# Kernel optimization log

Measured on AMD Instinct MI355X. Metric: run time of the kernel, lower is better.

## Reference

```python
import jax, jax.numpy as jnp
import numpy as np

M, K, N = 8192, 4096, 4096

def setup_inputs() -> dict:
    key = jax.random.key(0)
    k1, k2, k3, k4 = jax.random.split(key, 4)
    x = jax.random.normal(k1, (M, K), dtype=jnp.float32)
    # pre-quantized int8 weights [K, N] and per-output-channel scales [N]
    weight_q = jax.random.randint(k2, (K, N), -128, 128, dtype=jnp.int32).astype(jnp.int8)
    weight_scale = (jax.random.uniform(k3, (N,), dtype=jnp.float32) * 0.01 + 1e-4)
    bias = jax.random.normal(k4, (N,), dtype=jnp.float32) * 0.02
    return {"x": x, "weight_q": weight_q, "weight_scale": weight_scale, "bias": bias}

def reference(x, weight_q, weight_scale, bias):
    # dynamic per-row int8 quantization of activations
    max_vals = jnp.max(jnp.abs(x), axis=-1, keepdims=True)          # [M, 1]
    a_scale = jnp.maximum(max_vals / 127.0, 1e-8)                    # [M, 1]
    x_q = jnp.clip(jnp.round(x / a_scale), -128, 127).astype(jnp.int8)
    c = jnp.matmul(x_q.astype(jnp.float32), weight_q.astype(jnp.float32))  # [M, N]
    # dequantize: per-row activation scale * per-column weight scale
    c = c * a_scale * weight_scale[None, :]
    out = c.astype(x.dtype) + bias
    return out
```

## Files before the change

### kernel.cpp

```cpp
#include <hip/hip_runtime.h>


typedef int int32x4 __attribute__((ext_vector_type(4)));

#define TILE_BM 256
#define TILE_BN 256
#define TILE_BK 128

__device__ __forceinline__ void async_copy16(const void* g, void* l) {
    __builtin_amdgcn_global_load_lds(
        (const __attribute__((address_space(1))) unsigned int*)g,
        (__attribute__((address_space(3))) unsigned int*)l,
        16, 0, 0);
}

__device__ __forceinline__ int quant1(float x, float s) {
    float q = rintf(x / s);
    q = fminf(127.0f, fmaxf(-128.0f, q));
    return (int)q;
}

__global__ __launch_bounds__(256) void quant_kernel(
    const float* __restrict__ x, signed char* __restrict__ xq,
    float* __restrict__ ascale, int K)
{
    const int row = blockIdx.x;
    const int t = threadIdx.x;
    const float4* xr4 = (const float4*)(x + (size_t)row * K);

    float4 v[4];
    float mx = 0.0f;
#pragma unroll
    for (int i = 0; i < 4; ++i) {
        v[i] = xr4[i * 256 + t];
        mx = fmaxf(mx, fmaxf(fmaxf(fabsf(v[i].x), fabsf(v[i].y)),
                             fmaxf(fabsf(v[i].z), fabsf(v[i].w))));
    }
#pragma unroll
    for (int off = 32; off > 0; off >>= 1)
        mx = fmaxf(mx, __shfl_xor(mx, off, 64));
    __shared__ float wmax[4];
    if ((t & 63) == 0) wmax[t >> 6] = mx;
    __syncthreads();
    mx = fmaxf(fmaxf(wmax[0], wmax[1]), fmaxf(wmax[2], wmax[3]));

    const float s = fmaxf(mx / 127.0f, 1e-8f);
    if (t == 0) ascale[row] = s;

    int* xqr = (int*)(xq + (size_t)row * K);
#pragma unroll
    for (int i = 0; i < 4; ++i) {
        const int b0 = quant1(v[i].x, s);
        const int b1 = quant1(v[i].y, s);
        const int b2 = quant1(v[i].z, s);
        const int b3 = quant1(v[i].w, s);
        xqr[i * 256 + t] = (b0 & 255) | ((b1 & 255) << 8) | ((b2 & 255) << 16) | ((b3 & 255) << 24);
    }
}

__global__ __launch_bounds__(256) void transpose_pack_kernel(
    const int* __restrict__ Bq, signed char* __restrict__ Bt, int K, int N)
{
    __shared__ int lds[64 * 17];
    const int t = threadIdx.x;
    const int n0 = blockIdx.x * 64;
    const int k0 = blockIdx.y * 64;

    const int r = t >> 4;
    const int ncol = (t & 15) * 4;

    const int* src = Bq + (size_t)(k0 + 4 * r) * N + n0 + ncol;
    const int4 u0 = *(const int4*)(src);
    const int4 u1 = *(const int4*)(src + N);
    const int4 u2 = *(const int4*)(src + 2 * (size_t)N);
    const int4 u3 = *(const int4*)(src + 3 * (size_t)N);

    lds[(ncol + 0) * 17 + r] = (u0.x & 255) | ((u1.x & 255) << 8) | ((u2.x & 255) << 16) | ((u3.x & 255) << 24);
    lds[(ncol + 1) * 17 + r] = (u0.y & 255) | ((u1.y & 255) << 8) | ((u2.y & 255) << 16) | ((u3.y & 255) << 24);
    lds[(ncol + 2) * 17 + r] = (u0.z & 255) | ((u1.z & 255) << 8) | ((u2.z & 255) << 16) | ((u3.z & 255) << 24);
    lds[(ncol + 3) * 17 + r] = (u0.w & 255) | ((u1.w & 255) << 8) | ((u2.w & 255) << 16) | ((u3.w & 255) << 24);
    __syncthreads();

    const int nl = t >> 2, ch = t & 3;
    int o[4];
#pragma unroll
    for (int i = 0; i < 4; ++i) o[i] = lds[nl * 17 + ch * 4 + i];
    *(int32x4*)(Bt + (size_t)(n0 + nl) * K + k0 + ch * 16) = *(const int32x4*)o;
}


#define SBAR() do { asm volatile("" ::: "memory"); __builtin_amdgcn_s_barrier(); asm volatile("" ::: "memory"); } while (0)
#define LGKM0() asm volatile("s_waitcnt lgkmcnt(0)" ::: "memory")
#define VMCNT(n) asm volatile("s_waitcnt vmcnt(" #n ")" ::: "memory")

#define MFMA_Q(AF, MB, NB)                                                              \
    do {                                                                                \
        __builtin_amdgcn_s_setprio(1);                                                  \
        _Pragma("unroll") for (int mm = 0; mm < 4; ++mm) {                              \
            _Pragma("unroll") for (int nn = 0; nn < 2; ++nn) {                          \
                int32x4 v = acc[(MB) + mm][(NB) + nn];                                  \
                v = __builtin_amdgcn_mfma_i32_16x16x64_i8(AF[mm][0], b[(NB) + nn][0], v, 0, 0, 0); \
                v = __builtin_amdgcn_mfma_i32_16x16x64_i8(AF[mm][1], b[(NB) + nn][1], v, 0, 0, 0); \
                acc[(MB) + mm][(NB) + nn] = v;                                          \
            }                                                                           \
        }                                                                               \
        __builtin_amdgcn_s_setprio(0);                                                  \
    } while (0)

__global__ __launch_bounds__(512, 2) void gemm_i8_kernel(
    const signed char* __restrict__ Aq, const signed char* __restrict__ Bt,
    const float* __restrict__ ascale, const float* __restrict__ wscale,
    const float* __restrict__ bias, float* __restrict__ C,
    int M, int N, int K)
{
    __shared__ __align__(16) signed char smem[131072];

    const int t = threadIdx.x;
    const int lane = t & 63;
    const int w = t >> 6;
    const int wr = w >> 2;
    const int wc = w & 3;
    const int ml = lane & 15, kq = lane >> 4;
    const int lr = lane >> 3, l8 = lane & 7;

    const int nbx = gridDim.x;
    int bid = blockIdx.y * nbx + blockIdx.x;
    const int nwg = nbx * gridDim.y;
    if ((nwg & 7) == 0) bid = (bid & 7) * (nwg >> 3) + (bid >> 3);
    const int m0 = (bid / nbx) * TILE_BM;
    const int n0 = (bid % nbx) * TILE_BN;

    const int srow = w * 8 + lr;
    const int stoff = srow * 128 + l8 * 16;
    const signed char* gA = Aq + (size_t)(m0 + srow) * K + ((l8 ^ lr) << 4);
    const signed char* gB = Bt + (size_t)(n0 + srow) * K + ((l8 ^ lr) << 4);

    auto stage = [&](int slot, int op, int h, int tk) {
        signed char* l = smem + slot * 65536 + op * 32768 + h * 16384 + stoff;
        const signed char* g = (op ? gB : gA) + (size_t)(h * 128) * K + (size_t)tk * TILE_BK;
        async_copy16(g, l);
        async_copy16(g + (size_t)64 * K, l + 8192);
    };

    const int axor = (ml & 7) << 4;
    const int c0 = (kq * 16) ^ axor;
    const int c1 = (64 + kq * 16) ^ axor;
    const int aBase = (wr * 128 + ml) * 128;
    const int bBase = 32768 + (wc * 64 + ml) * 128;

    int32x4 acc[8][4] = {};
    int32x4 a0[4][2], a1[4][2], b[4][2];

    auto rdA = [&](int32x4 (&dst)[4][2], int slotoff, int mb) {
#pragma unroll
        for (int mm = 0; mm < 4; ++mm) {
            const signed char* p = smem + slotoff + aBase + (mb + mm) * 2048;
            dst[mm][0] = *(const int32x4*)(p + c0);
            dst[mm][1] = *(const int32x4*)(p + c1);
        }
    };
    auto rdB = [&](int slotoff) {
#pragma unroll
        for (int nn = 0; nn < 4; ++nn) {
            const signed char* p = smem + slotoff + bBase + nn * 2048;
            b[nn][0] = *(const int32x4*)(p + c0);
            b[nn][1] = *(const int32x4*)(p + c1);
        }
    };

    const int NI = K / (2 * TILE_BK);

    stage(0, 0, 0, 0); stage(0, 0, 1, 0); stage(0, 1, 0, 0); stage(0, 1, 1, 0);
    stage(1, 0, 0, 1); stage(1, 0, 1, 1);
    VMCNT(4);
    SBAR();

    for (int i = 0; i < NI; ++i) {
        const bool last = (i == NI - 1);
        const int t1 = 2 * i + 1, t2 = 2 * i + 2, t3 = 2 * i + 3;

        rdA(a0, 0, 0);
        rdB(0);
        stage(1, 1, 0, t1);
        SBAR();
        MFMA_Q(a0, 0, 0);
        LGKM0();
        SBAR();

        rdA(a1, 0, 4);
        stage(1, 1, 1, t1);
        SBAR();
        MFMA_Q(a0, 0, 2);
        LGKM0();
        SBAR();

        if (!last) stage(0, 0, 0, t2);
        SBAR();
        MFMA_Q(a1, 4, 0);
        SBAR();

        if (!last) { stage(0, 0, 1, t2); VMCNT(4); }
        else       { VMCNT(0); }
        SBAR();
        MFMA_Q(a1, 4, 2);
        SBAR();

        rdA(a0, 65536, 0);
        rdB(65536);
        if (!last) stage(0, 1, 0, t2);
        SBAR();
        MFMA_Q(a0, 0, 0);
        LGKM0();
        SBAR();

        rdA(a1, 65536, 4);
        if (!last) stage(0, 1, 1, t2);
        SBAR();
        MFMA_Q(a0, 0, 2);
        LGKM0();
        SBAR();

        if (!last) stage(1, 0, 0, t3);
        SBAR();
        MFMA_Q(a1, 4, 0);
        SBAR();

        if (!last) { stage(1, 0, 1, t3); VMCNT(4); }
        SBAR();
        MFMA_Q(a1, 4, 2);
        SBAR();
    }

    const int colb = n0 + wc * 64 + ml;
    const int rowb = m0 + wr * 128 + kq * 4;
#pragma unroll
    for (int n = 0; n < 4; ++n) {
        const int col = colb + n * 16;
        const float wsn = wscale[col];
        const float bsn = bias[col];
#pragma unroll
        for (int m = 0; m < 8; ++m) {
            const int row = rowb + m * 16;
            float* cp = C + (size_t)row * N + col;
#pragma unroll
            for (int r = 0; r < 4; ++r) {
                cp[(size_t)r * N] = ((float)acc[m][n][r] * ascale[row + r]) * wsn + bsn;
            }
        }
    }
}

extern "C" void kernel_launch(void* const* d_in, const int* in_sizes, int n_in,
                              void* d_out, int out_size, void* d_ws, size_t ws_size,
                              hipStream_t stream) {
    const float* x      = (const float*)d_in[0];
    const int*   wq     = (const int*)d_in[1];
    const float* wscale = (const float*)d_in[2];
    const float* bias   = (const float*)d_in[3];
    float* out          = (float*)d_out;

    const int N = in_sizes[2];
    const int K = in_sizes[1] / N;
    const int M = in_sizes[0] / K;

    char* ws = (char*)d_ws;
    signed char* xq = (signed char*)ws;
    signed char* bt = (signed char*)(ws + (size_t)M * K);
    float* ascale   = (float*)(ws + (size_t)M * K + (size_t)N * K);

    quant_kernel<<<M, 256, 0, stream>>>(x, xq, ascale, K);
    transpose_pack_kernel<<<dim3(N / 64, K / 64), 256, 0, stream>>>(wq, bt, K, N);
    gemm_i8_kernel<<<dim3(N / TILE_BN, M / TILE_BM), 512, 0, stream>>>(
        xq, bt, ascale, wscale, bias, out, M, N, K);
}
```

Baseline: 395.2 us.

## Merge prep kernels into one launch and software-pipeline LDS reads in GEMM loop

Fuses the activation quantization and weight transpose-pack kernels into a single launch whose blocks branch on blockIdx, removing one kernel launch and letting the two jobs run concurrently. It also restructures the GEMM main loop so fragment reads for the next MFMA group are issued before the current group executes. B fragments are now read in halves, the stage ordering changes, and the last iteration is peeled into an epilogue. The finer-grained interleaving is meant to hide LDS latency behind MFMA work, at the cost of more complex wait-count bookkeeping and a higher risk of races.

```diff
diff --git a/kernel.cpp b/kernel.cpp
--- a/kernel.cpp
+++ b/kernel.cpp
@@ -20,72 +20,72 @@
     return (int)q;
 }
 
-__global__ __launch_bounds__(256) void quant_kernel(
-    const float* __restrict__ x, signed char* __restrict__ xq,
-    float* __restrict__ ascale, int K)
+__global__ __launch_bounds__(256) void prep_kernel(
+    const float* __restrict__ x, signed char* __restrict__ xq, float* __restrict__ ascale,
+    const int* __restrict__ Bq, signed char* __restrict__ Bt, int K, int N, int M)
 {
-    const int row = blockIdx.x;
-    const int t = threadIdx.x;
-    const float4* xr4 = (const float4*)(x + (size_t)row * K);
-
-    float4 v[4];
-    float mx = 0.0f;
-#pragma unroll
-    for (int i = 0; i < 4; ++i) {
-        v[i] = xr4[i * 256 + t];
-        mx = fmaxf(mx, fmaxf(fmaxf(fabsf(v[i].x), fabsf(v[i].y)),
-                             fmaxf(fabsf(v[i].z), fabsf(v[i].w))));
-    }
-#pragma unroll
-    for (int off = 32; off > 0; off >>= 1)
-        mx = fmaxf(mx, __shfl_xor(mx, off, 64));
     __shared__ float wmax[4];
-    if ((t & 63) == 0) wmax[t >> 6] = mx;
-    __syncthreads();
-    mx = fmaxf(fmaxf(wmax[0], wmax[1]), fmaxf(wmax[2], wmax[3]));
-
-    const float s = fmaxf(mx / 127.0f, 1e-8f);
-    if (t == 0) ascale[row] = s;
-
-    int* xqr = (int*)(xq + (size_t)row * K);
-#pragma unroll
-    for (int i = 0; i < 4; ++i) {
-        const int b0 = quant1(v[i].x, s);
-        const int b1 = quant1(v[i].y, s);
-        const int b2 = quant1(v[i].z, s);
-        const int b3 = quant1(v[i].w, s);
-        xqr[i * 256 + t] = (b0 & 255) | ((b1 & 255) << 8) | ((b2 & 255) << 16) | ((b3 & 255) << 24);
-    }
-}
-
-__global__ __launch_bounds__(256) void transpose_pack_kernel(
-    const int* __restrict__ Bq, signed char* __restrict__ Bt, int K, int N)
-{
     __shared__ int lds[64 * 17];
     const int t = threadIdx.x;
-    const int n0 = blockIdx.x * 64;
-    const int k0 = blockIdx.y * 64;
-
-    const int r = t >> 4;
-    const int ncol = (t & 15) * 4;
-
-    const int* src = Bq + (size_t)(k0 + 4 * r) * N + n0 + ncol;
-    const int4 u0 = *(const int4*)(src);
-    const int4 u1 = *(const int4*)(src + N);
-    const int4 u2 = *(const int4*)(src + 2 * (size_t)N);
-    const int4 u3 = *(const int4*)(src + 3 * (size_t)N);
-
-    lds[(ncol + 0) * 17 + r] = (u0.x & 255) | ((u1.x & 255) << 8) | ((u2.x & 255) << 16) | ((u3.x & 255) << 24);
-    lds[(ncol + 1) * 17 + r] = (u0.y & 255) | ((u1.y & 255) << 8) | ((u2.y & 255) << 16) | ((u3.y & 255) << 24);
-    lds[(ncol + 2) * 17 + r] = (u0.z & 255) | ((u1.z & 255) << 8) | ((u2.z & 255) << 16) | ((u3.z & 255) << 24);
-    lds[(ncol + 3) * 17 + r] = (u0.w & 255) | ((u1.w & 255) << 8) | ((u2.w & 255) << 16) | ((u3.w & 255) << 24);
-    __syncthreads();
-
-    const int nl = t >> 2, ch = t & 3;
-    int o[4];
-#pragma unroll
-    for (int i = 0; i < 4; ++i) o[i] = lds[nl * 17 + ch * 4 + i];
-    *(int32x4*)(Bt + (size_t)(n0 + nl) * K + k0 + ch * 16) = *(const int32x4*)o;
+
+    if ((int)blockIdx.x < M) {
+        const int row = blockIdx.x;
+        const float4* xr4 = (const float4*)(x + (size_t)row * K);
+
+        float4 v[4];
+        float mx = 0.0f;
+#pragma unroll
+        for (int i = 0; i < 4; ++i) {
+            v[i] = xr4[i * 256 + t];
+            mx = fmaxf(mx, fmaxf(fmaxf(fabsf(v[i].x), fabsf(v[i].y)),
+                                 fmaxf(fabsf(v[i].z), fabsf(v[i].w))));
+        }
+#pragma unroll
+        for (int off = 32; off > 0; off >>= 1)
+            mx = fmaxf(mx, __shfl_xor(mx, off, 64));
+        if ((t & 63) == 0) wmax[t >> 6] = mx;
+        __syncthreads();
+        mx = fmaxf(fmaxf(wmax[0], wmax[1]), fmaxf(wmax[2], wmax[3]));
+
+        const float s = fmaxf(mx / 127.0f, 1e-8f);
+        if (t == 0) ascale[row] = s;
+
+        int* xqr = (int*)(xq + (size_t)row * K);
+#pragma unroll
+        for (int i = 0; i < 4; ++i) {
+            const int b0 = quant1(v[i].x, s);
+            const int b1 = quant1(v[i].y, s);
+            const int b2 = quant1(v[i].z, s);
+            const int b3 = quant1(v[i].w, s);
+            xqr[i * 256 + t] = (b0 & 255) | ((b1 & 255) << 8) | ((b2 & 255) << 16) | ((b3 & 255) << 24);
+        }
+    } else {
+        const int tb = (int)blockIdx.x - M;
+        const int nbx = N >> 6;
+        const int n0 = (tb % nbx) * 64;
+        const int k0 = (tb / nbx) * 64;
+
+        const int r = t >> 4;
+        const int ncol = (t & 15) * 4;
+
+        const int* src = Bq + (size_t)(k0 + 4 * r) * N + n0 + ncol;
+        const int4 u0 = *(const int4*)(src);
+        const int4 u1 = *(const int4*)(src + N);
+        const int4 u2 = *(const int4*)(src + 2 * (size_t)N);
+        const int4 u3 = *(const int4*)(src + 3 * (size_t)N);
+
+        lds[(ncol + 0) * 17 + r] = (u0.x & 255) | ((u1.x & 255) << 8) | ((u2.x & 255) << 16) | ((u3.x & 255) << 24);
+        lds[(ncol + 1) * 17 + r] = (u0.y & 255) | ((u1.y & 255) << 8) | ((u2.y & 255) << 16) | ((u3.y & 255) << 24);
+        lds[(ncol + 2) * 17 + r] = (u0.z & 255) | ((u1.z & 255) << 8) | ((u2.z & 255) << 16) | ((u3.z & 255) << 24);
+        lds[(ncol + 3) * 17 + r] = (u0.w & 255) | ((u1.w & 255) << 8) | ((u2.w & 255) << 16) | ((u3.w & 255) << 24);
+        __syncthreads();
+
+        const int nl = t >> 2, ch = t & 3;
+        int o[4];
+#pragma unroll
+        for (int i = 0; i < 4; ++i) o[i] = lds[nl * 17 + ch * 4 + i];
+        *(int32x4*)(Bt + (size_t)(n0 + nl) * K + k0 + ch * 16) = *(const int32x4*)o;
+    }
 }
 
 
@@ -159,76 +159,109 @@
             dst[mm][1] = *(const int32x4*)(p + c1);
         }
     };
-    auto rdB = [&](int slotoff) {
-#pragma unroll
-        for (int nn = 0; nn < 4; ++nn) {
-            const signed char* p = smem + slotoff + bBase + nn * 2048;
-            b[nn][0] = *(const int32x4*)(p + c0);
-            b[nn][1] = *(const int32x4*)(p + c1);
+    auto rdB2 = [&](int slotoff, int nb) {
+#pragma unroll
+        for (int nn = 0; nn < 2; ++nn) {
+            const signed char* p = smem + slotoff + bBase + (nb + nn) * 2048;
+            b[nb + nn][0] = *(const int32x4*)(p + c0);
+            b[nb + nn][1] = *(const int32x4*)(p + c1);
         }
     };
 
     const int NI = K / (2 * TILE_BK);
+    const int S0 = 0, S1 = 65536;
 
     stage(0, 0, 0, 0); stage(0, 0, 1, 0); stage(0, 1, 0, 0); stage(0, 1, 1, 0);
-    stage(1, 0, 0, 1); stage(1, 0, 1, 1);
+    stage(1, 1, 0, 1); stage(1, 1, 1, 1);
     VMCNT(4);
     SBAR();
-
-    for (int i = 0; i < NI; ++i) {
-        const bool last = (i == NI - 1);
+    rdA(a0, S0, 0);
+    rdB2(S0, 0);
+
+    for (int i = 0; i < NI - 1; ++i) {
         const int t1 = 2 * i + 1, t2 = 2 * i + 2, t3 = 2 * i + 3;
 
-        rdA(a0, 0, 0);
-        rdB(0);
-        stage(1, 1, 0, t1);
+        rdA(a1, S0, 4);
+        stage(1, 0, 0, t1);
         SBAR();
         MFMA_Q(a0, 0, 0);
+        SBAR();
+        rdB2(S0, 2);
+        stage(1, 0, 1, t1);
+        SBAR();
+        MFMA_Q(a1, 4, 0);
         LGKM0();
-        SBAR();
-
-        rdA(a1, 0, 4);
-        stage(1, 1, 1, t1);
+        VMCNT(4);
+        SBAR();
+        rdB2(S1, 0);
+        stage(0, 1, 0, t2);
         SBAR();
         MFMA_Q(a0, 0, 2);
+        VMCNT(2);
+        SBAR();
+        rdA(a0, S1, 0);
+        stage(0, 1, 1, t2);
+        SBAR();
+        MFMA_Q(a1, 4, 2);
+        SBAR();
+        rdA(a1, S1, 4);
+        stage(0, 0, 0, t2);
+        SBAR();
+        MFMA_Q(a0, 0, 0);
+        SBAR();
+        rdB2(S1, 2);
+        stage(0, 0, 1, t2);
+        SBAR();
+        MFMA_Q(a1, 4, 0);
         LGKM0();
-        SBAR();
-
-        if (!last) stage(0, 0, 0, t2);
+        VMCNT(4);
+        SBAR();
+        rdB2(S0, 0);
+        stage(1, 1, 0, t3);
+        SBAR();
+        MFMA_Q(a0, 0, 2);
+        VMCNT(2);
+        SBAR();
+        rdA(a0, S0, 0);
+        stage(1, 1, 1, t3);
+        SBAR();
+        MFMA_Q(a1, 4, 2);
+        SBAR();
+    }
+
+    {
+        const int t1 = 2 * NI - 1;
+        rdA(a1, S0, 4);
+        stage(1, 0, 0, t1);
+        SBAR();
+        MFMA_Q(a0, 0, 0);
+        SBAR();
+        rdB2(S0, 2);
+        stage(1, 0, 1, t1);
         SBAR();
         MFMA_Q(a1, 4, 0);
-        SBAR();
-
-        if (!last) { stage(0, 0, 1, t2); VMCNT(4); }
-        else       { VMCNT(0); }
+        VMCNT(4);
+        SBAR();
+        rdB2(S1, 0);
+        SBAR();
+        MFMA_Q(a0, 0, 2);
+        VMCNT(0);
+        SBAR();
+        rdA(a0, S1, 0);
         SBAR();
         MFMA_Q(a1, 4, 2);
         SBAR();
-
-        rdA(a0, 65536, 0);
-        rdB(65536);
-        if (!last) stage(0, 1, 0, t2);
+        rdA(a1, S1, 4);
         SBAR();
         MFMA_Q(a0, 0, 0);
-        LGKM0();
-        SBAR();
-
-        rdA(a1, 65536, 4);
-        if (!last) stage(0, 1, 1, t2);
+        SBAR();
+        rdB2(S1, 2);
+        SBAR();
+        MFMA_Q(a1, 4, 0);
         SBAR();
         MFMA_Q(a0, 0, 2);
-        LGKM0();
-        SBAR();
-
-        if (!last) stage(1, 0, 0, t3);
-        SBAR();
-        MFMA_Q(a1, 4, 0);
-        SBAR();
-
-        if (!last) { stage(1, 0, 1, t3); VMCNT(4); }
         SBAR();
         MFMA_Q(a1, 4, 2);
-        SBAR();
     }
 
     const int colb = n0 + wc * 64 + ml;
@@ -268,8 +301,8 @@
     signed char* bt = (signed char*)(ws + (size_t)M * K);
     float* ascale   = (float*)(ws + (size_t)M * K + (size_t)N * K);
 
-    quant_kernel<<<M, 256, 0, stream>>>(x, xq, ascale, K);
-    transpose_pack_kernel<<<dim3(N / 64, K / 64), 256, 0, stream>>>(wq, bt, K, N);
+    const int prepBlocks = M + (N >> 6) * (K >> 6);
+    prep_kernel<<<prepBlocks, 256, 0, stream>>>(x, xq, ascale, wq, bt, K, N, M);
     gemm_i8_kernel<<<dim3(N / TILE_BN, M / TILE_BM), 512, 0, stream>>>(
         xq, bt, ascale, wscale, bias, out, M, N, K);
 }
```

Measured after the change: 636.6 us. 1.61x slower.

## Restructure int8 GEMM main loop with split B fragments and peeled tail

Applied to the files above, without the earlier changes.

Reorganizes the register fragments into a single A buffer plus three half-width B buffers, reordering the eight MFMA quadrants so that LDS reads of the next fragments overlap with MFMAs on the current ones. B for the next tile is prefetched before the loop body ends, the stage order now loads B before A, and the final iteration is peeled so the loop no longer needs conditional staging. Launch bounds drop from two blocks per CU to one, freeing registers for the extra fragments but removing cross-block latency hiding. The tighter wait counts and barrier ordering carry a risk of subtle LDS race conditions.

```diff
diff --git a/kernel.cpp b/kernel.cpp
--- a/kernel.cpp
+++ b/kernel.cpp
@@ -93,21 +93,21 @@
 #define LGKM0() asm volatile("s_waitcnt lgkmcnt(0)" ::: "memory")
 #define VMCNT(n) asm volatile("s_waitcnt vmcnt(" #n ")" ::: "memory")
 
-#define MFMA_Q(AF, MB, NB)                                                              \
+#define MFMAQ(MB, BP, NB)                                                               \
     do {                                                                                \
         __builtin_amdgcn_s_setprio(1);                                                  \
         _Pragma("unroll") for (int mm = 0; mm < 4; ++mm) {                              \
             _Pragma("unroll") for (int nn = 0; nn < 2; ++nn) {                          \
                 int32x4 v = acc[(MB) + mm][(NB) + nn];                                  \
-                v = __builtin_amdgcn_mfma_i32_16x16x64_i8(AF[mm][0], b[(NB) + nn][0], v, 0, 0, 0); \
-                v = __builtin_amdgcn_mfma_i32_16x16x64_i8(AF[mm][1], b[(NB) + nn][1], v, 0, 0, 0); \
+                v = __builtin_amdgcn_mfma_i32_16x16x64_i8(a[mm][0], BP[nn][0], v, 0, 0, 0); \
+                v = __builtin_amdgcn_mfma_i32_16x16x64_i8(a[mm][1], BP[nn][1], v, 0, 0, 0); \
                 acc[(MB) + mm][(NB) + nn] = v;                                          \
             }                                                                           \
         }                                                                               \
         __builtin_amdgcn_s_setprio(0);                                                  \
     } while (0)
 
-__global__ __launch_bounds__(512, 2) void gemm_i8_kernel(
+__global__ __launch_bounds__(512, 1) void gemm_i8_kernel(
     const signed char* __restrict__ Aq, const signed char* __restrict__ Bt,
     const float* __restrict__ ascale, const float* __restrict__ wscale,
     const float* __restrict__ bias, float* __restrict__ C,
@@ -149,86 +149,120 @@
     const int bBase = 32768 + (wc * 64 + ml) * 128;
 
     int32x4 acc[8][4] = {};
-    int32x4 a0[4][2], a1[4][2], b[4][2];
-
-    auto rdA = [&](int32x4 (&dst)[4][2], int slotoff, int mb) {
+    int32x4 a[4][2], b01a[2][2], b01b[2][2], b23[2][2];
+
+    auto rdA = [&](int slotoff, int mb) {
 #pragma unroll
         for (int mm = 0; mm < 4; ++mm) {
             const signed char* p = smem + slotoff + aBase + (mb + mm) * 2048;
-            dst[mm][0] = *(const int32x4*)(p + c0);
-            dst[mm][1] = *(const int32x4*)(p + c1);
+            a[mm][0] = *(const int32x4*)(p + c0);
+            a[mm][1] = *(const int32x4*)(p + c1);
         }
     };
-    auto rdB = [&](int slotoff) {
-#pragma unroll
-        for (int nn = 0; nn < 4; ++nn) {
-            const signed char* p = smem + slotoff + bBase + nn * 2048;
-            b[nn][0] = *(const int32x4*)(p + c0);
-            b[nn][1] = *(const int32x4*)(p + c1);
+    auto rdB = [&](int32x4 (&dst)[2][2], int slotoff, int nb) {
+#pragma unroll
+        for (int nn = 0; nn < 2; ++nn) {
+            const signed char* p = smem + slotoff + bBase + (nb + nn) * 2048;
+            dst[nn][0] = *(const int32x4*)(p + c0);
+            dst[nn][1] = *(const int32x4*)(p + c1);
         }
     };
 
     const int NI = K / (2 * TILE_BK);
-
-    stage(0, 0, 0, 0); stage(0, 0, 1, 0); stage(0, 1, 0, 0); stage(0, 1, 1, 0);
-    stage(1, 0, 0, 1); stage(1, 0, 1, 1);
-    VMCNT(4);
+    const int S0 = 0, S1 = 65536;
+
+    stage(0, 1, 0, 0); stage(0, 1, 1, 0); stage(0, 0, 0, 0); stage(0, 0, 1, 0);
+    stage(1, 1, 0, 1);
+    VMCNT(2);
     SBAR();
-
-    for (int i = 0; i < NI; ++i) {
-        const bool last = (i == NI - 1);
+    rdB(b01a, S0, 0);
+
+    for (int i = 0; i < NI - 1; ++i) {
         const int t1 = 2 * i + 1, t2 = 2 * i + 2, t3 = 2 * i + 3;
 
-        rdA(a0, 0, 0);
-        rdB(0);
-        stage(1, 1, 0, t1);
-        SBAR();
-        MFMA_Q(a0, 0, 0);
+        rdA(S0, 0);
+        stage(1, 1, 1, t1);
+        SBAR(); LGKM0();
+        MFMAQ(0, b01a, 0);
+        SBAR();
+        rdB(b23, S0, 2);
+        stage(1, 0, 0, t1);
+        SBAR(); LGKM0();
+        MFMAQ(0, b23, 2);
+        SBAR();
+        rdA(S0, 4);
+        stage(1, 0, 1, t1);
+        SBAR(); LGKM0();
+        MFMAQ(4, b23, 2);
+        VMCNT(4);
+        SBAR();
+        rdB(b01b, S1, 0);
+        stage(0, 1, 0, t2);
+        SBAR();
+        MFMAQ(4, b01a, 0);
+        VMCNT(2);
+        SBAR();
+        rdA(S1, 0);
+        stage(0, 1, 1, t2);
+        SBAR(); LGKM0();
+        MFMAQ(0, b01b, 0);
+        SBAR();
+        rdB(b23, S1, 2);
+        stage(0, 0, 0, t2);
+        SBAR(); LGKM0();
+        MFMAQ(0, b23, 2);
+        SBAR();
+        rdA(S1, 4);
+        stage(0, 0, 1, t2);
+        SBAR(); LGKM0();
+        MFMAQ(4, b23, 2);
+        VMCNT(4);
+        SBAR();
+        rdB(b01a, S0, 0);
+        stage(1, 1, 0, t3);
+        SBAR();
+        MFMAQ(4, b01b, 0);
+        VMCNT(2);
+        SBAR();
+    }
+
+    {
+        const int t1 = 2 * NI - 1;
+        rdA(S0, 0);
+        stage(1, 1, 1, t1);
+        SBAR(); LGKM0();
+        MFMAQ(0, b01a, 0);
+        SBAR();
+        rdB(b23, S0, 2);
+        stage(1, 0, 0, t1);
+        SBAR(); LGKM0();
+        MFMAQ(0, b23, 2);
+        SBAR();
+        rdA(S0, 4);
+        stage(1, 0, 1, t1);
+        SBAR(); LGKM0();
+        MFMAQ(4, b23, 2);
+        VMCNT(4);
+        SBAR();
+        rdB(b01b, S1, 0);
+        SBAR();
+        MFMAQ(4, b01a, 0);
+        VMCNT(0);
+        SBAR();
+        rdA(S1, 0);
+        SBAR(); LGKM0();
+        MFMAQ(0, b01b, 0);
+        SBAR();
+        rdB(b23, S1, 2);
+        SBAR(); LGKM0();
+        MFMAQ(0, b23, 2);
+        SBAR();
+        rdA(S1, 4);
+        SBAR(); LGKM0();
+        MFMAQ(4, b23, 2);
+        SBAR();
         LGKM0();
-        SBAR();
-
-        rdA(a1, 0, 4);
-        stage(1, 1, 1, t1);
-        SBAR();
-        MFMA_Q(a0, 0, 2);
-        LGKM0();
-        SBAR();
-
-        if (!last) stage(0, 0, 0, t2);
-        SBAR();
-        MFMA_Q(a1, 4, 0);
-        SBAR();
-
-        if (!last) { stage(0, 0, 1, t2); VMCNT(4); }
-        else       { VMCNT(0); }
-        SBAR();
-        MFMA_Q(a1, 4, 2);
-        SBAR();
-
-        rdA(a0, 65536, 0);
-        rdB(65536);
-        if (!last) stage(0, 1, 0, t2);
-        SBAR();
-        MFMA_Q(a0, 0, 0);
-        LGKM0();
-        SBAR();
-
-        rdA(a1, 65536, 4);
-        if (!last) stage(0, 1, 1, t2);
-        SBAR();
-        MFMA_Q(a0, 0, 2);
-        LGKM0();
-        SBAR();
-
-        if (!last) stage(1, 0, 0, t3);
-        SBAR();
-        MFMA_Q(a1, 4, 0);
-        SBAR();
-
-        if (!last) { stage(1, 0, 1, t3); VMCNT(4); }
-        SBAR();
-        MFMA_Q(a1, 4, 2);
-        SBAR();
+        MFMAQ(4, b01b, 0);
     }
 
     const int colb = n0 + wc * 64 + ml;
```

Result: no change. 389.5 us (-1.4%).

## Restructure int8 GEMM main loop into K-half phases with fewer barriers

Applied to the files above, without the earlier changes.

Replaces the eight-phase main loop, which had a barrier and lgkmcnt wait around every MFMA quarter, with a simpler schedule. Each 128-wide K tile is split into two 64-wide halves, and LDS fragment reads for the next half are interleaved with MFMAs on the current one. Whole tiles are prefetched into the other LDS slot with a single vmcnt(0) plus barrier per tile. Launch bounds drop to one block per CU; the 128 KB LDS footprint already limits occupancy to one block, so this mainly frees registers. The cost is a shallower prefetch window per tile and reliance on the compiler to place LDS waits correctly.

```diff
diff --git a/kernel.cpp b/kernel.cpp
--- a/kernel.cpp
+++ b/kernel.cpp
@@ -90,24 +90,19 @@
 
 
 #define SBAR() do { asm volatile("" ::: "memory"); __builtin_amdgcn_s_barrier(); asm volatile("" ::: "memory"); } while (0)
-#define LGKM0() asm volatile("s_waitcnt lgkmcnt(0)" ::: "memory")
 #define VMCNT(n) asm volatile("s_waitcnt vmcnt(" #n ")" ::: "memory")
 
-#define MFMA_Q(AF, MB, NB)                                                              \
+#define MFMAQ(AB, BB, MB)                                                               \
     do {                                                                                \
         __builtin_amdgcn_s_setprio(1);                                                  \
-        _Pragma("unroll") for (int mm = 0; mm < 4; ++mm) {                              \
-            _Pragma("unroll") for (int nn = 0; nn < 2; ++nn) {                          \
-                int32x4 v = acc[(MB) + mm][(NB) + nn];                                  \
-                v = __builtin_amdgcn_mfma_i32_16x16x64_i8(AF[mm][0], b[(NB) + nn][0], v, 0, 0, 0); \
-                v = __builtin_amdgcn_mfma_i32_16x16x64_i8(AF[mm][1], b[(NB) + nn][1], v, 0, 0, 0); \
-                acc[(MB) + mm][(NB) + nn] = v;                                          \
-            }                                                                           \
-        }                                                                               \
+        _Pragma("unroll") for (int mm = 0; mm < 4; ++mm)                                \
+            _Pragma("unroll") for (int nn = 0; nn < 4; ++nn)                            \
+                acc[(MB) + mm][nn] = __builtin_amdgcn_mfma_i32_16x16x64_i8(             \
+                    AB[mm], BB[nn], acc[(MB) + mm][nn], 0, 0, 0);                       \
         __builtin_amdgcn_s_setprio(0);                                                  \
     } while (0)
 
-__global__ __launch_bounds__(512, 2) void gemm_i8_kernel(
+__global__ __launch_bounds__(512, 1) void gemm_i8_kernel(
     const signed char* __restrict__ Aq, const signed char* __restrict__ Bt,
     const float* __restrict__ ascale, const float* __restrict__ wscale,
     const float* __restrict__ bias, float* __restrict__ C,
@@ -141,6 +136,10 @@
         async_copy16(g, l);
         async_copy16(g + (size_t)64 * K, l + 8192);
     };
+    auto stage_tile = [&](int slot, int tk) {
+        stage(slot, 0, 0, tk); stage(slot, 0, 1, tk);
+        stage(slot, 1, 0, tk); stage(slot, 1, 1, tk);
+    };
 
     const int axor = (ml & 7) << 4;
     const int c0 = (kq * 16) ^ axor;
@@ -149,86 +148,54 @@
     const int bBase = 32768 + (wc * 64 + ml) * 128;
 
     int32x4 acc[8][4] = {};
-    int32x4 a0[4][2], a1[4][2], b[4][2];
-
-    auto rdA = [&](int32x4 (&dst)[4][2], int slotoff, int mb) {
+    int32x4 A0[4], A1[4], B0[4], B1[4];
+
+    auto rdA4 = [&](int32x4 (&dst)[4], int slotoff, int mb, int kc) {
 #pragma unroll
         for (int mm = 0; mm < 4; ++mm) {
             const signed char* p = smem + slotoff + aBase + (mb + mm) * 2048;
-            dst[mm][0] = *(const int32x4*)(p + c0);
-            dst[mm][1] = *(const int32x4*)(p + c1);
+            dst[mm] = *(const int32x4*)(p + kc);
         }
     };
-    auto rdB = [&](int slotoff) {
+    auto rdB4 = [&](int32x4 (&dst)[4], int slotoff, int kc) {
 #pragma unroll
         for (int nn = 0; nn < 4; ++nn) {
             const signed char* p = smem + slotoff + bBase + nn * 2048;
-            b[nn][0] = *(const int32x4*)(p + c0);
-            b[nn][1] = *(const int32x4*)(p + c1);
+            dst[nn] = *(const int32x4*)(p + kc);
         }
     };
 
-    const int NI = K / (2 * TILE_BK);
-
-    stage(0, 0, 0, 0); stage(0, 0, 1, 0); stage(0, 1, 0, 0); stage(0, 1, 1, 0);
-    stage(1, 0, 0, 1); stage(1, 0, 1, 1);
-    VMCNT(4);
+    const int NT = K / TILE_BK;
+    const int S0 = 0, S1 = 65536;
+
+    stage_tile(0, 0);
+    stage_tile(1, 1);
+    VMCNT(8);
     SBAR();
 
-    for (int i = 0; i < NI; ++i) {
-        const bool last = (i == NI - 1);
-        const int t1 = 2 * i + 1, t2 = 2 * i + 2, t3 = 2 * i + 3;
-
-        rdA(a0, 0, 0);
-        rdB(0);
-        stage(1, 1, 0, t1);
+    for (int i = 0; i < NT / 2; ++i) {
+        rdA4(A0, S0, 0, c0); rdB4(B0, S0, c0);
+        rdA4(A1, S0, 4, c0);
+        if (i > 0) stage_tile(1, 2 * i + 1);
+        MFMAQ(A0, B0, 0);
+        rdA4(A0, S0, 0, c1); rdB4(B1, S0, c1);
+        MFMAQ(A1, B0, 4);
+        rdA4(A1, S0, 4, c1);
+        MFMAQ(A0, B1, 0);
+        MFMAQ(A1, B1, 4);
+        VMCNT(0);
         SBAR();
-        MFMA_Q(a0, 0, 0);
-        LGKM0();
-        SBAR();
-
-        rdA(a1, 0, 4);
-        stage(1, 1, 1, t1);
-        SBAR();
-        MFMA_Q(a0, 0, 2);
-        LGKM0();
-        SBAR();
-
-        if (!last) stage(0, 0, 0, t2);
-        SBAR();
-        MFMA_Q(a1, 4, 0);
-        SBAR();
-
-        if (!last) { stage(0, 0, 1, t2); VMCNT(4); }
-        else       { VMCNT(0); }
-        SBAR();
-        MFMA_Q(a1, 4, 2);
-        SBAR();
-
-        rdA(a0, 65536, 0);
-        rdB(65536);
-        if (!last) stage(0, 1, 0, t2);
-        SBAR();
-        MFMA_Q(a0, 0, 0);
-        LGKM0();
-        SBAR();
-
-        rdA(a1, 65536, 4);
-        if (!last) stage(0, 1, 1, t2);
-        SBAR();
-        MFMA_Q(a0, 0, 2);
-        LGKM0();
-        SBAR();
-
-        if (!last) stage(1, 0, 0, t3);
-        SBAR();
-        MFMA_Q(a1, 4, 0);
-        SBAR();
-
-        if (!last) { stage(1, 0, 1, t3); VMCNT(4); }
-        SBAR();
-        MFMA_Q(a1, 4, 2);
-        SBAR();
+
+        rdA4(A0, S1, 0, c0); rdB4(B0, S1, c0);
+        rdA4(A1, S1, 4, c0);
+        if (i < NT / 2 - 1) stage_tile(0, 2 * i + 2);
+        MFMAQ(A0, B0, 0);
+        rdA4(A0, S1, 0, c1); rdB4(B1, S1, c1);
+        MFMAQ(A1, B0, 4);
+        rdA4(A1, S1, 4, c1);
+        MFMAQ(A0, B1, 0);
+        MFMAQ(A1, B1, 4);
+        if (i < NT / 2 - 1) { VMCNT(0); SBAR(); }
     }
 
     const int colb = n0 + wc * 64 + ml;
```

After: 434.9 us. 10.1% more time.
